# Optimization experiments

Measured on AMD Instinct MI355X. Metric: run time of the kernel, lower is better.

Reference implementation:

```python
import jax, jax.numpy as jnp
from jax import lax
import numpy as np

B, IN_DIM, T, L, CONN = 32, 256, 512, 512, 256
LN_EPS = 1e-3  # keras LayerNormalization default


def setup_inputs() -> dict:
    key = jax.random.key(0)
    ks = jax.random.split(key, 16)
    g = lambda k, shape, fan: jax.random.normal(k, shape, jnp.float32) * (2.0 / sum(fan)) ** 0.5
    return {
        "x": jax.random.normal(ks[0], (B, IN_DIM, T), jnp.float32),
        "connectivity": jax.random.normal(ks[1], (B, T, CONN), jnp.float32),
        # RandomFourierFeatures: trainable projection + bias, layer-normalized cos features
        "Wf": g(ks[2], (IN_DIM, L), (IN_DIM, L)),
        "bf": jax.random.uniform(ks[3], (L,), jnp.float32, 0.0, 2.0 * np.pi),
        "gamma": jnp.ones((L,), jnp.float32),
        "beta": jnp.zeros((L,), jnp.float32),
        # input gate
        "Wi": g(ks[4], (L, L), (L, L)),
        "Ri": g(ks[5], (L, L), (L, L)),
        "bi": jnp.zeros((L,), jnp.float32),
        # forget gate
        "Wg": g(ks[6], (L, L), (L, L)),
        "Rg": g(ks[7], (L, L), (L, L)),
        "bg": jnp.zeros((L,), jnp.float32),
        # connectivity Dense projection
        "Wc": g(ks[8], (CONN, L), (CONN, L)),
        "bc": jnp.zeros((L,), jnp.float32),
        # learned initial states (stored squeezed to [L])
        "init_h": g(ks[9], (L,), (1, L)),
        "init_c": g(ks[10], (L,), (1, L)),
    }


def reference(x, connectivity, Wf, bf, gamma, beta, Wi, Ri, bi, Wg, Rg, bg, Wc, bc, init_h, init_c):
    xt = jnp.transpose(x, (0, 2, 1))                      # [B, T, in_dim]
    # random fourier features with layer normalization
    p = jnp.cos(xt @ Wf + bf)                             # [B, T, L]
    mu = jnp.mean(p, axis=-1, keepdims=True)
    var = jnp.var(p, axis=-1, keepdims=True)
    z = gamma * (p - mu) * lax.rsqrt(var + LN_EPS) + beta

    o = jnp.sin(z)                                        # sinusoid output gate
    u = connectivity @ Wc + bc                            # [B, T, L] connectivity injection

    b = x.shape[0]
    # hidden_states[t+1] = z_t in the original, so the recurrent term at step t is z_{t-1}
    h0 = jnp.broadcast_to(init_h, (b, 1, z.shape[-1]))
    z_prev = jnp.concatenate([h0, z[:, :-1, :]], axis=1)  # [B, T, L]

    i = jax.nn.sigmoid(z @ Wi + z_prev @ Ri + bi)
    f = jax.nn.sigmoid(z @ Wg + z_prev @ Rg + bg)
    iu = i * u

    def step(c, fi):
        ft, iut = fi
        c = ft * c + iut
        return c, c

    c0 = jnp.broadcast_to(init_c, (b, z.shape[-1]))
    _, cs = lax.scan(step, c0, (jnp.moveaxis(f, 1, 0), jnp.moveaxis(iu, 1, 0)))
    cs = jnp.moveaxis(cs, 0, 1)                           # [B, T, L]
    h = o * cs
    return jnp.transpose(h, (0, 2, 1))                    # [B, L, T]
```

## Files before the change

### kernel.cpp

```cpp
#include <hip/hip_runtime.h>
#include <hip/hip_bf16.h>

#define NB 32
#define IN_DIM 256
#define NT 512
#define NL 512
#define NCONN 256
#define LN_EPS 1e-3f
#define M_TOT (NB * NT)

typedef __attribute__((ext_vector_type(8))) short short8;
typedef __attribute__((ext_vector_type(4))) float f32x4;

__device__ __forceinline__ void async_copy16(void* lds_dst, const void* g_src) {
    __builtin_amdgcn_global_load_lds(
        (const __attribute__((address_space(1))) unsigned int*)g_src,
        (__attribute__((address_space(3))) unsigned int*)lds_dst, 16, 0, 0);
}

__global__ __launch_bounds__(256) void xprep_transpose(
    const float* __restrict__ x, __hip_bfloat16* __restrict__ Axt)
{
    __shared__ float t[64][65];
    const int tilesPerB = (IN_DIM / 64) * (NT / 64);
    const int b  = blockIdx.x / tilesPerB;
    const int tl = blockIdx.x % tilesPerB;
    const int k0 = (tl / (NT / 64)) * 64;
    const int t0 = (tl % (NT / 64)) * 64;
    const int tid = threadIdx.x;
    const float* src = x + (size_t)b * IN_DIM * NT;
    for (int idx = tid; idx < 4096; idx += 256) {
        const int kk = idx >> 6, tt = idx & 63;
        t[kk][tt] = src[(size_t)(k0 + kk) * NT + t0 + tt];
    }
    __syncthreads();
    for (int idx = tid; idx < 4096; idx += 256) {
        const int tt = idx >> 6, kk = idx & 63;
        Axt[((size_t)b * NT + t0 + tt) * IN_DIM + k0 + kk] =
            __float2bfloat16(t[kk][tt]);
    }
}

__global__ void fill_ihb(const float* __restrict__ init_h,
                         __hip_bfloat16* __restrict__ ihb)
{
    const int l = threadIdx.x;
    ihb[l] = __float2bfloat16(init_h[l]);
}

__global__ __launch_bounds__(512, 2) void k1_mfma_fourier_ln(
    const __hip_bfloat16* __restrict__ Axt,
    const __hip_bfloat16* __restrict__ WfT,
    const float* __restrict__ bf, const float* __restrict__ gamma,
    const float* __restrict__ beta,
    __hip_bfloat16* __restrict__ zb)
{
    constexpr int ABYTES = 64 * 128;
    constexpr int BBYTES = 512 * 128;
    constexpr int NBUFB  = ABYTES + BBYTES;
    __shared__ __align__(16) char lds[2 * NBUFB];
    __shared__ float pS[64][8], pQ[64][8];
    __shared__ float mS[64], rS[64];

    const int tid  = threadIdx.x;
    const int wave = tid >> 6, lane = tid & 63;
    const int m0 = blockIdx.x * 64;

    f32x4 acc[4][4];
#pragma unroll
    for (int mi = 0; mi < 4; mi++)
#pragma unroll
        for (int ni = 0; ni < 4; ni++) acc[mi][ni] = f32x4{0.f, 0.f, 0.f, 0.f};

    const int rowq = tid >> 3;
    const int sswz = ((tid & 7) ^ (rowq & 7)) << 4;
    const char* Ab = (const char*)Axt;
    const char* Bb = (const char*)WfT;

    auto stage = [&](int buf, int kt) {
        const size_t kb = (size_t)kt * 128;
        char* base = lds + buf * NBUFB;
        async_copy16(base + tid * 16,
                     Ab + (size_t)(m0 + rowq) * 512 + kb + sswz);
#pragma unroll
        for (int j = 0; j < 8; j++) {
            const int row = j * 64 + rowq;
            async_copy16(base + ABYTES + (j * 512 + tid) * 16,
                         Bb + (size_t)row * 512 + kb + sswz);
        }
    };

    const int l15 = lane & 15, lq = lane >> 4, l7 = lane & 7;
    int kxB[2];
#pragma unroll
    for (int ks = 0; ks < 2; ks++) kxB[ks] = ((ks * 4 + lq) ^ l7) << 4;

    stage(0, 0);
    int cur = 0;
#pragma unroll 1
    for (int kt = 0; kt < 4; kt++) {
        __syncthreads();
        if (kt + 1 < 4) stage(cur ^ 1, kt + 1);
        const char* sA = lds + cur * NBUFB;
        const char* sB = sA + ABYTES;
#pragma unroll
        for (int ks = 0; ks < 2; ks++) {
            const int kx = kxB[ks];
            short8 a[4], b[4];
#pragma unroll
            for (int mi = 0; mi < 4; mi++)
                a[mi] = *(const short8*)(sA + (size_t)(mi * 16 + l15) * 128 + kx);
#pragma unroll
            for (int ni = 0; ni < 4; ni++)
                b[ni] = *(const short8*)(sB +
                    (size_t)(wave * 64 + ni * 16 + l15) * 128 + kx);
#pragma unroll
            for (int ni = 0; ni < 4; ni++)
#pragma unroll
                for (int mi = 0; mi < 4; mi++)
                    acc[mi][ni] = __builtin_amdgcn_mfma_f32_16x16x32_bf16(
                        a[mi], b[ni], acc[mi][ni], 0, 0, 0);
        }
        cur ^= 1;
    }

    int cg[4]; float bfc[4];
#pragma unroll
    for (int ni = 0; ni < 4; ni++) {
        cg[ni] = wave * 64 + ni * 16 + l15;
        bfc[ni] = bf[cg[ni]];
    }

#pragma unroll
    for (int mi = 0; mi < 4; mi++) {
#pragma unroll
        for (int r = 0; r < 4; r++) {
            float s = 0.f, q = 0.f;
#pragma unroll
            for (int ni = 0; ni < 4; ni++) {
                const float p = __cosf(acc[mi][ni][r] + bfc[ni]);
                s += p; q += p * p;
            }
#pragma unroll
            for (int off = 8; off >= 1; off >>= 1) {
                s += __shfl_xor(s, off);
                q += __shfl_xor(q, off);
            }
            if (l15 == 0) {
                const int row = mi * 16 + lq * 4 + r;
                pS[row][wave] = s;
                pQ[row][wave] = q;
            }
        }
    }
    __syncthreads();
    if (tid < 64) {
        float a = 0.f, qq = 0.f;
#pragma unroll
        for (int w = 0; w < 8; w++) { a += pS[tid][w]; qq += pQ[tid][w]; }
        const float mu = a * (1.0f / NL);
        const float var = qq * (1.0f / NL) - mu * mu;
        mS[tid] = mu;
        rS[tid] = rsqrtf(var + LN_EPS);
    }
    __syncthreads();

    float gm[4], bt[4];
#pragma unroll
    for (int ni = 0; ni < 4; ni++) { gm[ni] = gamma[cg[ni]]; bt[ni] = beta[cg[ni]]; }

#pragma unroll
    for (int mi = 0; mi < 4; mi++) {
#pragma unroll
        for (int r = 0; r < 4; r++) {
            const int row = mi * 16 + lq * 4 + r;
            const int m = m0 + row;
            const float mu = mS[row], rs = rS[row];
#pragma unroll
            for (int ni = 0; ni < 4; ni++) {
                const float p = __cosf(acc[mi][ni][r] + bfc[ni]);
                const float z = gm[ni] * (p - mu) * rs + bt[ni];
                zb[(size_t)m * 512 + cg[ni]] = __float2bfloat16(z);
            }
        }
    }
}

__global__ __launch_bounds__(256) void wconv_transpose(
    const float* __restrict__ src, __hip_bfloat16* __restrict__ dst,
    int K, int N, int lddst, int k_off)
{
    __shared__ float t[64][65];
    const int ntn = N >> 6;
    const int k0 = (blockIdx.x / ntn) << 6;
    const int n0 = (blockIdx.x % ntn) << 6;
    const int tid = threadIdx.x;
    for (int idx = tid; idx < 4096; idx += 256) {
        const int kk = idx >> 6, nn = idx & 63;
        t[kk][nn] = src[(size_t)(k0 + kk) * N + n0 + nn];
    }
    __syncthreads();
    for (int idx = tid; idx < 4096; idx += 256) {
        const int nn = idx >> 6, kk = idx & 63;
        dst[(size_t)(n0 + nn) * lddst + k_off + k0 + kk] = __float2bfloat16(t[kk][nn]);
    }
}

__global__ __launch_bounds__(256) void conv_bf16_vec(
    const float* __restrict__ src, __hip_bfloat16* __restrict__ dst, int n)
{
    const int e = (blockIdx.x * 256 + threadIdx.x) * 4;
    if (e < n) {
        const float4 v = *(const float4*)(src + e);
        dst[e + 0] = __float2bfloat16(v.x);
        dst[e + 1] = __float2bfloat16(v.y);
        dst[e + 2] = __float2bfloat16(v.z);
        dst[e + 3] = __float2bfloat16(v.w);
    }
}

template<int KTOT, int EPI>
__global__ __launch_bounds__(256, 2) void gemm128(
    const __hip_bfloat16* __restrict__ A,
    const __hip_bfloat16* __restrict__ B,
    const __hip_bfloat16* __restrict__ ihb,
    const float* __restrict__ bi, const float* __restrict__ bg,
    const float* __restrict__ bc,
    __hip_bfloat16* __restrict__ fb, __hip_bfloat16* __restrict__ ub)
{
    constexpr int NTN = (EPI == 1) ? 8 : 4;
    constexpr int TB  = KTOT / 64;
    __shared__ __align__(16) char lds[2][32768];

    const int tid  = threadIdx.x;
    const int wave = tid >> 6, lane = tid & 63;
    const int wm = wave >> 1, wn = wave & 1;
    constexpr int CPX = 128 * NTN / 8;
    const int d = blockIdx.x;
    const int L = (d & 7) * CPX + (d >> 3);
    const int m0 = (L / NTN) << 7;
    const int n0 = (L % NTN) << 7;

    f32x4 acc[4][4];
#pragma unroll
    for (int mi = 0; mi < 4; mi++)
#pragma unroll
        for (int ni = 0; ni < 4; ni++) acc[mi][ni] = f32x4{0.f, 0.f, 0.f, 0.f};

    auto stage = [&](int buf, int kt) {
        char* base = &lds[buf][0];
#pragma unroll
        for (int j = 0; j < 4; j++) {
            const int i = j * 256 + tid;
            const int r = i >> 3;
            const int sl = (i & 7) ^ (r & 7);
            const int ke = kt * 64 + sl * 8;
            const __hip_bfloat16* srcA;
            if constexpr (EPI == 1) {
                const int m = m0 + r;
                if (ke < 512) {
                    srcA = A + (size_t)m * 512 + ke;
                } else {
                    const int k2 = ke - 512;
                    srcA = ((m & (NT - 1)) == 0) ? (ihb + k2)
                                                 : (A + (size_t)(m - 1) * 512 + k2);
                }
            } else {
                srcA = A + (size_t)(m0 + r) * KTOT + ke;
            }
            async_copy16(base + i * 16, srcA);
            async_copy16(base + 16384 + i * 16,
                         B + (size_t)(n0 + r) * KTOT + ke);
        }
    };

    const int l15 = lane & 15, lq = lane >> 4, l7 = lane & 7;
    int kx[2];
#pragma unroll
    for (int ks = 0; ks < 2; ks++) kx[ks] = ((ks * 4 + lq) ^ l7) << 4;

    stage(0, 0);
    int cur = 0;
#pragma unroll 1
    for (int kt = 0; kt < TB; kt++) {
        __syncthreads();
        if (kt + 1 < TB) stage(cur ^ 1, kt + 1);
        const char* sA = &lds[cur][0];
        const char* sB = &lds[cur][16384];
#pragma unroll
        for (int ks = 0; ks < 2; ks++) {
            short8 a[4], b[4];
#pragma unroll
            for (int mi = 0; mi < 4; mi++)
                a[mi] = *(const short8*)(sA +
                    (size_t)(wm * 64 + mi * 16 + l15) * 128 + kx[ks]);
#pragma unroll
            for (int ni = 0; ni < 4; ni++)
                b[ni] = *(const short8*)(sB +
                    (size_t)(wn * 64 + ni * 16 + l15) * 128 + kx[ks]);
#pragma unroll
            for (int ni = 0; ni < 4; ni++)
#pragma unroll
                for (int mi = 0; mi < 4; mi++)
                    acc[mi][ni] = __builtin_amdgcn_mfma_f32_16x16x32_bf16(
                        a[mi], b[ni], acc[mi][ni], 0, 0, 0);
        }
        cur ^= 1;
    }

#pragma unroll
    for (int ni = 0; ni < 4; ni++) {
        const int gcol = n0 + wn * 64 + ni * 16 + l15;
        if constexpr (EPI == 0) {
            const float bcl = bc[gcol];
#pragma unroll
            for (int mi = 0; mi < 4; mi++)
#pragma unroll
                for (int r = 0; r < 4; r++) {
                    const int m = m0 + wm * 64 + mi * 16 + lq * 4 + r;
                    ub[(size_t)m * 512 + gcol] =
                        __float2bfloat16(acc[mi][ni][r] + bcl);
                }
        } else {
            if (gcol < 512) {
                const float bil = bi[gcol];
#pragma unroll
                for (int mi = 0; mi < 4; mi++)
#pragma unroll
                    for (int r = 0; r < 4; r++) {
                        const int m = m0 + wm * 64 + mi * 16 + lq * 4 + r;
                        const size_t idx = (size_t)m * 512 + gcol;
                        const float iv =
                            1.f / (1.f + __expf(-(acc[mi][ni][r] + bil)));
                        const float uv = __bfloat162float(ub[idx]);
                        ub[idx] = __float2bfloat16(iv * uv);
                    }
            } else {
                const int l2 = gcol - 512;
                const float bgl = bg[l2];
#pragma unroll
                for (int mi = 0; mi < 4; mi++)
#pragma unroll
                    for (int r = 0; r < 4; r++) {
                        const int m = m0 + wm * 64 + mi * 16 + lq * 4 + r;
                        const float fv =
                            1.f / (1.f + __expf(-(acc[mi][ni][r] + bgl)));
                        fb[(size_t)m * 512 + l2] = __float2bfloat16(fv);
                    }
            }
        }
    }
}

__global__ __launch_bounds__(64) void k3_scan(
    const __hip_bfloat16* __restrict__ zb,
    const __hip_bfloat16* __restrict__ fb,
    const __hip_bfloat16* __restrict__ ub,
    const float* __restrict__ init_c, float* __restrict__ out)
{
    const int b = blockIdx.x >> 3;
    const int l = ((blockIdx.x & 7) << 6) + threadIdx.x;
    float c = init_c[l];

    const __hip_bfloat16* zp = zb + (size_t)b * NT * 512 + l;
    const __hip_bfloat16* fp = fb + (size_t)b * NT * NL + l;
    const __hip_bfloat16* ip = ub + (size_t)b * NT * NL + l;
    float* op = out + ((size_t)b * NL + l) * NT;

    for (int t0 = 0; t0 < NT; t0 += 16) {
        float fv[16], iv[16], zv[16];
#pragma unroll
        for (int j = 0; j < 16; j++) {
            fv[j] = __bfloat162float(fp[(size_t)(t0 + j) * NL]);
            iv[j] = __bfloat162float(ip[(size_t)(t0 + j) * NL]);
            zv[j] = __bfloat162float(zp[(size_t)(t0 + j) * 512]);
        }
        float h[16];
#pragma unroll
        for (int j = 0; j < 16; j++) {
            c = fv[j] * c + iv[j];
            h[j] = __sinf(zv[j]) * c;
        }
        float4* o4 = (float4*)(op + t0);
        o4[0] = make_float4(h[0],  h[1],  h[2],  h[3]);
        o4[1] = make_float4(h[4],  h[5],  h[6],  h[7]);
        o4[2] = make_float4(h[8],  h[9],  h[10], h[11]);
        o4[3] = make_float4(h[12], h[13], h[14], h[15]);
    }
}

extern "C" void kernel_launch(void* const* d_in, const int* in_sizes, int n_in,
                              void* d_out, int out_size, void* d_ws, size_t ws_size,
                              hipStream_t stream)
{
    const float* x      = (const float*)d_in[0];
    const float* conn   = (const float*)d_in[1];
    const float* Wf     = (const float*)d_in[2];
    const float* bfv    = (const float*)d_in[3];
    const float* gamma  = (const float*)d_in[4];
    const float* beta   = (const float*)d_in[5];
    const float* Wi     = (const float*)d_in[6];
    const float* Ri     = (const float*)d_in[7];
    const float* bi     = (const float*)d_in[8];
    const float* Wg     = (const float*)d_in[9];
    const float* Rg     = (const float*)d_in[10];
    const float* bg     = (const float*)d_in[11];
    const float* Wc     = (const float*)d_in[12];
    const float* bc     = (const float*)d_in[13];
    const float* init_h = (const float*)d_in[14];
    const float* init_c = (const float*)d_in[15];

    char* w = (char*)d_ws;
    __hip_bfloat16* zbuf = (__hip_bfloat16*)w;  w += (size_t)M_TOT * 512 * 2;
    __hip_bfloat16* cbuf = (__hip_bfloat16*)w;  w += (size_t)M_TOT * NCONN * 2;
    __hip_bfloat16* fbuf = (__hip_bfloat16*)w;  w += (size_t)M_TOT * NL * 2;
    __hip_bfloat16* ubuf = (__hip_bfloat16*)w;  w += (size_t)M_TOT * NL * 2;
    __hip_bfloat16* xbuf = (__hip_bfloat16*)w;  w += (size_t)M_TOT * IN_DIM * 2;
    __hip_bfloat16* WfT  = (__hip_bfloat16*)w;  w += (size_t)NL * IN_DIM * 2;
    __hip_bfloat16* Btig = (__hip_bfloat16*)w;  w += (size_t)1024 * 1024 * 2;
    __hip_bfloat16* Btc  = (__hip_bfloat16*)w;  w += (size_t)NL * NCONN * 2;
    __hip_bfloat16* ihb  = (__hip_bfloat16*)w;  w += 512 * 2;

    wconv_transpose<<<32, 256, 0, stream>>>(Wf, WfT, 256, 512, 256, 0);
    wconv_transpose<<<64, 256, 0, stream>>>(Wi, Btig, 512, 512, 1024, 0);
    wconv_transpose<<<64, 256, 0, stream>>>(Ri, Btig, 512, 512, 1024, 512);
    wconv_transpose<<<64, 256, 0, stream>>>(Wg, Btig + (size_t)512 * 1024, 512, 512, 1024, 0);
    wconv_transpose<<<64, 256, 0, stream>>>(Rg, Btig + (size_t)512 * 1024, 512, 512, 1024, 512);
    wconv_transpose<<<32, 256, 0, stream>>>(Wc, Btc, 256, 512, 256, 0);
    conv_bf16_vec<<<(M_TOT * NCONN / 4 + 255) / 256, 256, 0, stream>>>(
        conn, cbuf, M_TOT * NCONN);
    xprep_transpose<<<NB * 32, 256, 0, stream>>>(x, xbuf);
    fill_ihb<<<1, 512, 0, stream>>>(init_h, ihb);

    k1_mfma_fourier_ln<<<M_TOT / 64, 512, 0, stream>>>(
        xbuf, WfT, bfv, gamma, beta, zbuf);

    gemm128<NCONN, 0><<<M_TOT / 128 * 4, 256, 0, stream>>>(
        cbuf, Btc, nullptr, nullptr, nullptr, bc, nullptr, ubuf);

    gemm128<1024, 1><<<M_TOT / 128 * 8, 256, 0, stream>>>(
        zbuf, Btig, ihb, bi, bg, nullptr, fbuf, ubuf);

    k3_scan<<<NB * 8, 64, 0, stream>>>(zbuf, fbuf, ubuf, init_c, (float*)d_out);
}
```

Measured before the change: 135.3 us.

## Enlarge GEMM tiles to 256x128 and drop LDS double buffering

The two MFMA GEMM kernels now compute 256x128 output tiles per block, with 8x4 accumulator fragments per wave, instead of 128x128. This halves the grid size and raises reuse of each B tile. To fit LDS, the ping-pong double buffer is replaced by a single buffer, with a barrier before and after each k-step. The change cuts global traffic and per-block overhead, but it loses the overlap of loads with compute, doubles accumulator register use (which may limit occupancy), and leaves fewer blocks to spread across CUs.

```diff
diff --git a/kernel.cpp b/kernel.cpp
--- a/kernel.cpp
+++ b/kernel.cpp
@@ -220,7 +220,7 @@
 }
 
 template<int KTOT, int EPI>
-__global__ __launch_bounds__(256, 2) void gemm128(
+__global__ __launch_bounds__(256, 2) void gemm256(
     const __hip_bfloat16* __restrict__ A,
     const __hip_bfloat16* __restrict__ B,
     const __hip_bfloat16* __restrict__ ihb,
@@ -230,27 +230,27 @@
 {
     constexpr int NTN = (EPI == 1) ? 8 : 4;
     constexpr int TB  = KTOT / 64;
-    __shared__ __align__(16) char lds[2][32768];
+    constexpr int ABYTES = 256 * 64 * 2;
+    __shared__ __align__(16) char lds[ABYTES + 128 * 64 * 2];
 
     const int tid  = threadIdx.x;
     const int wave = tid >> 6, lane = tid & 63;
     const int wm = wave >> 1, wn = wave & 1;
-    constexpr int CPX = 128 * NTN / 8;
+    constexpr int CPX = 64 * NTN / 8;
     const int d = blockIdx.x;
     const int L = (d & 7) * CPX + (d >> 3);
-    const int m0 = (L / NTN) << 7;
+    const int m0 = (L / NTN) << 8;
     const int n0 = (L % NTN) << 7;
 
-    f32x4 acc[4][4];
-#pragma unroll
-    for (int mi = 0; mi < 4; mi++)
+    f32x4 acc[8][4];
+#pragma unroll
+    for (int mi = 0; mi < 8; mi++)
 #pragma unroll
         for (int ni = 0; ni < 4; ni++) acc[mi][ni] = f32x4{0.f, 0.f, 0.f, 0.f};
 
-    auto stage = [&](int buf, int kt) {
-        char* base = &lds[buf][0];
-#pragma unroll
-        for (int j = 0; j < 4; j++) {
+    auto stage = [&](int kt) {
+#pragma unroll
+        for (int j = 0; j < 8; j++) {
             const int i = j * 256 + tid;
             const int r = i >> 3;
             const int sl = (i & 7) ^ (r & 7);
@@ -268,8 +268,15 @@
             } else {
                 srcA = A + (size_t)(m0 + r) * KTOT + ke;
             }
-            async_copy16(base + i * 16, srcA);
-            async_copy16(base + 16384 + i * 16,
+            async_copy16(lds + i * 16, srcA);
+        }
+#pragma unroll
+        for (int j = 0; j < 4; j++) {
+            const int i = j * 256 + tid;
+            const int r = i >> 3;
+            const int sl = (i & 7) ^ (r & 7);
+            const int ke = kt * 64 + sl * 8;
+            async_copy16(lds + ABYTES + i * 16,
                          B + (size_t)(n0 + r) * KTOT + ke);
         }
     };
@@ -279,21 +286,19 @@
 #pragma unroll
     for (int ks = 0; ks < 2; ks++) kx[ks] = ((ks * 4 + lq) ^ l7) << 4;
 
-    stage(0, 0);
-    int cur = 0;
 #pragma unroll 1
     for (int kt = 0; kt < TB; kt++) {
+        stage(kt);
         __syncthreads();
-        if (kt + 1 < TB) stage(cur ^ 1, kt + 1);
-        const char* sA = &lds[cur][0];
-        const char* sB = &lds[cur][16384];
+        const char* sA = lds;
+        const char* sB = lds + ABYTES;
 #pragma unroll
         for (int ks = 0; ks < 2; ks++) {
-            short8 a[4], b[4];
-#pragma unroll
-            for (int mi = 0; mi < 4; mi++)
+            short8 a[8], b[4];
+#pragma unroll
+            for (int mi = 0; mi < 8; mi++)
                 a[mi] = *(const short8*)(sA +
-                    (size_t)(wm * 64 + mi * 16 + l15) * 128 + kx[ks]);
+                    (size_t)(wm * 128 + mi * 16 + l15) * 128 + kx[ks]);
 #pragma unroll
             for (int ni = 0; ni < 4; ni++)
                 b[ni] = *(const short8*)(sB +
@@ -301,11 +306,11 @@
 #pragma unroll
             for (int ni = 0; ni < 4; ni++)
 #pragma unroll
-                for (int mi = 0; mi < 4; mi++)
+                for (int mi = 0; mi < 8; mi++)
                     acc[mi][ni] = __builtin_amdgcn_mfma_f32_16x16x32_bf16(
                         a[mi], b[ni], acc[mi][ni], 0, 0, 0);
         }
-        cur ^= 1;
+        __syncthreads();
     }
 
 #pragma unroll
@@ -314,10 +319,10 @@
         if constexpr (EPI == 0) {
             const float bcl = bc[gcol];
 #pragma unroll
-            for (int mi = 0; mi < 4; mi++)
+            for (int mi = 0; mi < 8; mi++)
 #pragma unroll
                 for (int r = 0; r < 4; r++) {
-                    const int m = m0 + wm * 64 + mi * 16 + lq * 4 + r;
+                    const int m = m0 + wm * 128 + mi * 16 + lq * 4 + r;
                     ub[(size_t)m * 512 + gcol] =
                         __float2bfloat16(acc[mi][ni][r] + bcl);
                 }
@@ -325,10 +330,10 @@
             if (gcol < 512) {
                 const float bil = bi[gcol];
 #pragma unroll
-                for (int mi = 0; mi < 4; mi++)
+                for (int mi = 0; mi < 8; mi++)
 #pragma unroll
                     for (int r = 0; r < 4; r++) {
-                        const int m = m0 + wm * 64 + mi * 16 + lq * 4 + r;
+                        const int m = m0 + wm * 128 + mi * 16 + lq * 4 + r;
                         const size_t idx = (size_t)m * 512 + gcol;
                         const float iv =
                             1.f / (1.f + __expf(-(acc[mi][ni][r] + bil)));
@@ -339,10 +344,10 @@
                 const int l2 = gcol - 512;
                 const float bgl = bg[l2];
 #pragma unroll
-                for (int mi = 0; mi < 4; mi++)
+                for (int mi = 0; mi < 8; mi++)
 #pragma unroll
                     for (int r = 0; r < 4; r++) {
-                        const int m = m0 + wm * 64 + mi * 16 + lq * 4 + r;
+                        const int m = m0 + wm * 128 + mi * 16 + lq * 4 + r;
                         const float fv =
                             1.f / (1.f + __expf(-(acc[mi][ni][r] + bgl)));
                         fb[(size_t)m * 512 + l2] = __float2bfloat16(fv);
@@ -435,10 +440,10 @@
     k1_mfma_fourier_ln<<<M_TOT / 64, 512, 0, stream>>>(
         xbuf, WfT, bfv, gamma, beta, zbuf);
 
-    gemm128<NCONN, 0><<<M_TOT / 128 * 4, 256, 0, stream>>>(
+    gemm256<NCONN, 0><<<M_TOT / 256 * 4, 256, 0, stream>>>(
         cbuf, Btc, nullptr, nullptr, nullptr, bc, nullptr, ubuf);
 
-    gemm128<1024, 1><<<M_TOT / 128 * 8, 256, 0, stream>>>(
+    gemm256<1024, 1><<<M_TOT / 256 * 8, 256, 0, stream>>>(
         zbuf, Btig, ihb, bi, bg, nullptr, fbuf, ubuf);
 
     k3_scan<<<NB * 8, 64, 0, stream>>>(zbuf, fbuf, ubuf, init_c, (float*)d_out);
```

New measurement: 137.4 us. No clear change (+1.5%).

## Replace gate GEMM with 256x256-tile, 8-wave kernel using phased staging

Applied to the files above, without the earlier changes.

The gate GEMM (z and z_prev against the concatenated Wi/Ri/Wg/Rg weights) moves to a dedicated kernel. It uses 256x256 output tiles, 512 threads and 64KB double-buffered LDS per stage. Each K-step is split into four phases whose async loads for the next tile are interleaved with MFMA bursts, using explicit vmcnt waits, barriers and setprio. The aim is better data reuse per tile and hiding global-load latency behind compute, at the cost of more LDS and registers per block, fewer blocks (256), and extra barriers. The connectivity GEMM is specialized into its own non-templated kernel.

```diff
diff --git a/kernel.cpp b/kernel.cpp
--- a/kernel.cpp
+++ b/kernel.cpp
@@ -219,27 +219,23 @@
     }
 }
 
-template<int KTOT, int EPI>
-__global__ __launch_bounds__(256, 2) void gemm128(
+__global__ __launch_bounds__(256, 2) void gemm_u(
     const __hip_bfloat16* __restrict__ A,
     const __hip_bfloat16* __restrict__ B,
-    const __hip_bfloat16* __restrict__ ihb,
-    const float* __restrict__ bi, const float* __restrict__ bg,
     const float* __restrict__ bc,
-    __hip_bfloat16* __restrict__ fb, __hip_bfloat16* __restrict__ ub)
-{
-    constexpr int NTN = (EPI == 1) ? 8 : 4;
-    constexpr int TB  = KTOT / 64;
+    __hip_bfloat16* __restrict__ ub)
+{
+    constexpr int KTOT = 256;
+    constexpr int TB = KTOT / 64;
     __shared__ __align__(16) char lds[2][32768];
 
     const int tid  = threadIdx.x;
     const int wave = tid >> 6, lane = tid & 63;
     const int wm = wave >> 1, wn = wave & 1;
-    constexpr int CPX = 128 * NTN / 8;
     const int d = blockIdx.x;
-    const int L = (d & 7) * CPX + (d >> 3);
-    const int m0 = (L / NTN) << 7;
-    const int n0 = (L % NTN) << 7;
+    const int L = (d & 7) * 64 + (d >> 3);
+    const int m0 = (L >> 2) << 7;
+    const int n0 = (L & 3) << 7;
 
     f32x4 acc[4][4];
 #pragma unroll
@@ -255,22 +251,8 @@
             const int r = i >> 3;
             const int sl = (i & 7) ^ (r & 7);
             const int ke = kt * 64 + sl * 8;
-            const __hip_bfloat16* srcA;
-            if constexpr (EPI == 1) {
-                const int m = m0 + r;
-                if (ke < 512) {
-                    srcA = A + (size_t)m * 512 + ke;
-                } else {
-                    const int k2 = ke - 512;
-                    srcA = ((m & (NT - 1)) == 0) ? (ihb + k2)
-                                                 : (A + (size_t)(m - 1) * 512 + k2);
-                }
-            } else {
-                srcA = A + (size_t)(m0 + r) * KTOT + ke;
-            }
-            async_copy16(base + i * 16, srcA);
-            async_copy16(base + 16384 + i * 16,
-                         B + (size_t)(n0 + r) * KTOT + ke);
+            async_copy16(base + i * 16, A + (size_t)(m0 + r) * KTOT + ke);
+            async_copy16(base + 16384 + i * 16, B + (size_t)(n0 + r) * KTOT + ke);
         }
     };
 
@@ -311,43 +293,154 @@
 #pragma unroll
     for (int ni = 0; ni < 4; ni++) {
         const int gcol = n0 + wn * 64 + ni * 16 + l15;
-        if constexpr (EPI == 0) {
-            const float bcl = bc[gcol];
-#pragma unroll
-            for (int mi = 0; mi < 4; mi++)
+        const float bcl = bc[gcol];
+#pragma unroll
+        for (int mi = 0; mi < 4; mi++)
+#pragma unroll
+            for (int r = 0; r < 4; r++) {
+                const int m = m0 + wm * 64 + mi * 16 + lq * 4 + r;
+                ub[(size_t)m * 512 + gcol] =
+                    __float2bfloat16(acc[mi][ni][r] + bcl);
+            }
+    }
+}
+
+__global__ __launch_bounds__(512, 2) void gates8ph(
+    const __hip_bfloat16* __restrict__ Az,
+    const __hip_bfloat16* __restrict__ B,
+    const __hip_bfloat16* __restrict__ ihb,
+    const float* __restrict__ bi, const float* __restrict__ bg,
+    __hip_bfloat16* __restrict__ fb, __hip_bfloat16* __restrict__ ub)
+{
+    constexpr int T = 16;
+    __shared__ __align__(16) char lds[2][65536];
+
+    const int tid  = threadIdx.x;
+    const int wave = tid >> 6, lane = tid & 63;
+    const int wm = wave >> 2, wn = wave & 3;
+    const int d = blockIdx.x;
+    const int L = ((d & 7) << 5) | (d >> 3);
+    const int m0 = (L >> 2) << 8;
+    const int n0 = (L & 3) << 8;
+
+    f32x4 acc[8][4];
+#pragma unroll
+    for (int mi = 0; mi < 8; mi++)
+#pragma unroll
+        for (int ni = 0; ni < 4; ni++) acc[mi][ni] = f32x4{0.f, 0.f, 0.f, 0.f};
+
+    const int l15 = lane & 15, lq = lane >> 4, l7 = lane & 7;
+    const int kx0 = (lq ^ l7) << 4;
+    const int kx1 = ((4 + lq) ^ l7) << 4;
+
+    auto stage_half = [&](int buf, int kt, int half) {
+#pragma unroll
+        for (int j = 0; j < 2; j++) {
+            const int i = j * 512 + tid;
+            const int r = i >> 3;
+            const int sl = (i & 7) ^ (r & 7);
+            const int ke = kt * 64 + sl * 8;
+            const __hip_bfloat16* src;
+            if (half < 2) {
+                const int m = m0 + half * 128 + r;
+                if (ke < 512) {
+                    src = Az + (size_t)m * 512 + ke;
+                } else {
+                    const int k2 = ke - 512;
+                    src = ((m & (NT - 1)) == 0) ? (ihb + k2)
+                                                : (Az + (size_t)(m - 1) * 512 + k2);
+                }
+            } else {
+                const int nr = n0 + (half - 2) * 128 + r;
+                src = B + (size_t)nr * 1024 + ke;
+            }
+            const int region = (half < 2) ? half * 16384
+                                          : 32768 + (half - 2) * 16384;
+            async_copy16(&lds[buf][region + i * 16], src);
+        }
+    };
+
+    stage_half(0, 0, 0); stage_half(0, 0, 1);
+    stage_half(0, 0, 2); stage_half(0, 0, 3);
+
+    int p = 0;
+#pragma unroll 1
+    for (int t = 0; t < T; t++) {
+        const int q = p ^ 1;
+        const bool st = (t + 1 < T);
+        if (st) {
+            stage_half(q, t + 1, 0);
+            asm volatile("s_waitcnt vmcnt(2)" ::: "memory");
+        } else {
+            asm volatile("s_waitcnt vmcnt(0)" ::: "memory");
+        }
+        __builtin_amdgcn_sched_barrier(0);
+        __builtin_amdgcn_s_barrier();
+        const char* bufp = lds[p];
+        short8 b_[4];
+
+#define GPHASE(MH, KXS, READB, DOSTAGE, STHALF)                               \
+        {                                                                     \
+            short8 a_[4];                                                     \
+            _Pragma("unroll")                                                 \
+            for (int mi = 0; mi < 4; mi++)                                    \
+                a_[mi] = *(const short8*)(bufp +                              \
+                    (size_t)(wm * 128 + MH * 64 + mi * 16 + l15) * 128 + KXS);\
+            if (READB) {                                                      \
+                _Pragma("unroll")                                             \
+                for (int ni = 0; ni < 4; ni++)                                \
+                    b_[ni] = *(const short8*)(bufp + 32768 +                  \
+                        (size_t)(wn * 64 + ni * 16 + l15) * 128 + KXS);       \
+            }                                                                 \
+            if (DOSTAGE) stage_half(q, t + 1, STHALF);                        \
+            __builtin_amdgcn_s_barrier();                                     \
+            __builtin_amdgcn_s_setprio(1);                                    \
+            _Pragma("unroll")                                                 \
+            for (int ni = 0; ni < 4; ni++)                                    \
+                _Pragma("unroll")                                             \
+                for (int mi = 0; mi < 4; mi++)                                \
+                    acc[MH * 4 + mi][ni] =                                    \
+                        __builtin_amdgcn_mfma_f32_16x16x32_bf16(              \
+                            a_[mi], b_[ni], acc[MH * 4 + mi][ni], 0, 0, 0);   \
+            __builtin_amdgcn_s_setprio(0);                                    \
+            __builtin_amdgcn_s_barrier();                                     \
+        }
+
+        GPHASE(0, kx0, true,  st, 1)
+        GPHASE(1, kx0, false, st, 2)
+        GPHASE(0, kx1, true,  st, 3)
+        GPHASE(1, kx1, false, false, 0)
+#undef GPHASE
+        p = q;
+    }
+
+#pragma unroll
+    for (int ni = 0; ni < 4; ni++) {
+        const int gcol = n0 + wn * 64 + ni * 16 + l15;
+        if (n0 < 512) {
+            const float bil = bi[gcol];
+#pragma unroll
+            for (int mi = 0; mi < 8; mi++)
 #pragma unroll
                 for (int r = 0; r < 4; r++) {
-                    const int m = m0 + wm * 64 + mi * 16 + lq * 4 + r;
-                    ub[(size_t)m * 512 + gcol] =
-                        __float2bfloat16(acc[mi][ni][r] + bcl);
+                    const int m = m0 + wm * 128 + mi * 16 + lq * 4 + r;
+                    const size_t idx = (size_t)m * 512 + gcol;
+                    const float iv =
+                        1.f / (1.f + __expf(-(acc[mi][ni][r] + bil)));
+                    ub[idx] = __float2bfloat16(iv * __bfloat162float(ub[idx]));
                 }
         } else {
-            if (gcol < 512) {
-                const float bil = bi[gcol];
-#pragma unroll
-                for (int mi = 0; mi < 4; mi++)
-#pragma unroll
-                    for (int r = 0; r < 4; r++) {
-                        const int m = m0 + wm * 64 + mi * 16 + lq * 4 + r;
-                        const size_t idx = (size_t)m * 512 + gcol;
-                        const float iv =
-                            1.f / (1.f + __expf(-(acc[mi][ni][r] + bil)));
-                        const float uv = __bfloat162float(ub[idx]);
-                        ub[idx] = __float2bfloat16(iv * uv);
-                    }
-            } else {
-                const int l2 = gcol - 512;
-                const float bgl = bg[l2];
-#pragma unroll
-                for (int mi = 0; mi < 4; mi++)
-#pragma unroll
-                    for (int r = 0; r < 4; r++) {
-                        const int m = m0 + wm * 64 + mi * 16 + lq * 4 + r;
-                        const float fv =
-                            1.f / (1.f + __expf(-(acc[mi][ni][r] + bgl)));
-                        fb[(size_t)m * 512 + l2] = __float2bfloat16(fv);
-                    }
-            }
+            const int g2 = gcol - 512;
+            const float bgl = bg[g2];
+#pragma unroll
+            for (int mi = 0; mi < 8; mi++)
+#pragma unroll
+                for (int r = 0; r < 4; r++) {
+                    const int m = m0 + wm * 128 + mi * 16 + lq * 4 + r;
+                    const float fv =
+                        1.f / (1.f + __expf(-(acc[mi][ni][r] + bgl)));
+                    fb[(size_t)m * 512 + g2] = __float2bfloat16(fv);
+                }
         }
     }
 }
@@ -435,11 +528,9 @@
     k1_mfma_fourier_ln<<<M_TOT / 64, 512, 0, stream>>>(
         xbuf, WfT, bfv, gamma, beta, zbuf);
 
-    gemm128<NCONN, 0><<<M_TOT / 128 * 4, 256, 0, stream>>>(
-        cbuf, Btc, nullptr, nullptr, nullptr, bc, nullptr, ubuf);
-
-    gemm128<1024, 1><<<M_TOT / 128 * 8, 256, 0, stream>>>(
-        zbuf, Btig, ihb, bi, bg, nullptr, fbuf, ubuf);
+    gemm_u<<<M_TOT / 128 * 4, 256, 0, stream>>>(cbuf, Btc, bc, ubuf);
+
+    gates8ph<<<256, 512, 0, stream>>>(zbuf, Btig, ihb, bi, bg, fbuf, ubuf);
 
     k3_scan<<<NB * 8, 64, 0, stream>>>(zbuf, fbuf, ubuf, init_c, (float*)d_out);
 }
```

Measured after the change: 137.2 us. About the same (+1.4%).
